# Optimization experiments

Hardware: AMD Instinct MI355X
Metric: run time of the kernel (lower is better)

## Reference

```python
import jax, jax.numpy as jnp
import numpy as np

B = 32; H = 56; W = 56; C = 384; NH = 12; WS = 7; SS = 3
N = WS * WS            # tokens per window = 49
NW = (H // WS) * (W // WS)  # windows per image = 64
HD = C // NH           # head dim = 32
MLP_H = 4 * C
EPS = 1e-5


def _rel_pos_index():
    coords = np.stack(np.meshgrid(np.arange(WS), np.arange(WS), indexing='ij'))
    cf = coords.reshape(2, -1)                      # (2, N)
    rel = cf[:, :, None] - cf[:, None, :]           # (2, N, N)
    rel = rel.transpose(1, 2, 0).astype(np.int64)   # (N, N, 2)
    rel[..., 0] += WS - 1
    rel[..., 1] += WS - 1
    rel[..., 0] *= 2 * WS - 1
    return rel.sum(-1)                               # (N, N)


def _attn_mask():
    img = np.zeros((H, W))
    cnt = 0
    slc = (slice(0, -WS), slice(-WS, -SS), slice(-SS, None))
    for hs in slc:
        for ws in slc:
            img[hs, ws] = cnt
            cnt += 1
    mw = img.reshape(H // WS, WS, W // WS, WS).transpose(0, 2, 1, 3).reshape(-1, N)  # (NW, N)
    diff = mw[:, None, :] - mw[:, :, None]
    return np.where(diff != 0, -100.0, 0.0).astype(np.float32)  # (NW, N, N)


_RPI = jnp.asarray(_rel_pos_index())
_MASK = jnp.asarray(_attn_mask())


def _ln(x, w, b):
    m = jnp.mean(x, axis=-1, keepdims=True)
    v = jnp.mean((x - m) ** 2, axis=-1, keepdims=True)
    return (x - m) * jax.lax.rsqrt(v + EPS) * w + b


def _window_partition(x):  # (B,H,W,C) -> (B*NW, WS, WS, C)
    x = x.reshape(B, H // WS, WS, W // WS, WS, C)
    return x.transpose(0, 1, 3, 2, 4, 5).reshape(-1, WS, WS, C)


def _window_reverse(xw):  # (B*NW, WS, WS, C) -> (B,H,W,C)
    x = xw.reshape(B, H // WS, W // WS, WS, WS, C)
    return x.transpose(0, 1, 3, 2, 4, 5).reshape(B, H, W, C)


def setup_inputs() -> dict:
    key = jax.random.key(0)
    ks = jax.random.split(key, 8)
    s = 0.02
    return {
        'x': jax.random.normal(ks[0], (B, H * W, C), jnp.float32),
        'norm1_w': jnp.ones((C,), jnp.float32),
        'norm1_b': jnp.zeros((C,), jnp.float32),
        'qkv_w': jax.random.normal(ks[1], (C, 3 * C), jnp.float32) * s,
        'qkv_b': jnp.zeros((3 * C,), jnp.float32),
        'rpb_table': jax.random.normal(ks[2], ((2 * WS - 1) * (2 * WS - 1), NH), jnp.float32) * s,
        'proj_w': jax.random.normal(ks[3], (C, C), jnp.float32) * s,
        'proj_b': jnp.zeros((C,), jnp.float32),
        'norm2_w': jnp.ones((C,), jnp.float32),
        'norm2_b': jnp.zeros((C,), jnp.float32),
        'fc1_w': jax.random.normal(ks[4], (C, MLP_H), jnp.float32) * s,
        'fc1_b': jnp.zeros((MLP_H,), jnp.float32),
        'fc2_w': jax.random.normal(ks[5], (MLP_H, C), jnp.float32) * s,
        'fc2_b': jnp.zeros((C,), jnp.float32),
    }


def reference(x, norm1_w, norm1_b, qkv_w, qkv_b, rpb_table, proj_w, proj_b,
              norm2_w, norm2_b, fc1_w, fc1_b, fc2_w, fc2_b):
    shortcut = x
    xn = _ln(x, norm1_w, norm1_b).reshape(B, H, W, C)
    # cyclic shift
    xs = jnp.roll(xn, shift=(-SS, -SS), axis=(1, 2))
    xw = _window_partition(xs).reshape(-1, N, C)           # (B*NW, N, C)

    qkv = (xw @ qkv_w + qkv_b).reshape(-1, N, 3, NH, HD)
    qkv = qkv.transpose(2, 0, 3, 1, 4)                      # (3, B*NW, NH, N, HD)
    q, k, v = qkv[0], qkv[1], qkv[2]
    q = q * (HD ** -0.5)
    attn = jnp.einsum('bhnd,bhmd->bhnm', q, k)              # (B*NW, NH, N, N)

    bias = rpb_table[_RPI.reshape(-1)].reshape(N, N, NH).transpose(2, 0, 1)
    attn = attn + bias[None]
    # shift mask: (NW, N, N) broadcast over batch and heads
    attn = attn.reshape(B, NW, NH, N, N) + _MASK[None, :, None]
    attn = jax.nn.softmax(attn.reshape(-1, NH, N, N), axis=-1)

    out = jnp.einsum('bhnm,bhmd->bhnd', attn, v)            # (B*NW, NH, N, HD)
    out = out.transpose(0, 2, 1, 3).reshape(-1, N, C)
    out = out @ proj_w + proj_b

    out = _window_reverse(out.reshape(-1, WS, WS, C))
    out = jnp.roll(out, shift=(SS, SS), axis=(1, 2)).reshape(B, H * W, C)

    x = shortcut + out
    h = _ln(x, norm2_w, norm2_b)
    h = jax.nn.gelu(h @ fc1_w + fc1_b, approximate=False) @ fc2_w + fc2_b
    return x + h
```

## Files before the change

### kernel.cpp

```cpp
#include <hip/hip_runtime.h>
#include <hip/hip_bf16.h>
#include <math.h>


typedef short bf16x8 __attribute__((ext_vector_type(8)));
typedef float f32x4 __attribute__((ext_vector_type(4)));

#define GLOAD_LDS16(g, s)                                                      \
    __builtin_amdgcn_global_load_lds(                                          \
        (const __attribute__((address_space(1))) void*)(g),                    \
        (__attribute__((address_space(3))) void*)(s), 16, 0, 0)

__global__ __launch_bounds__(256) void prep_k(
    const float* __restrict__ qkvw, const float* __restrict__ projw,
    const float* __restrict__ fc1w, const float* __restrict__ fc2w,
    const float* __restrict__ rpb,
    __hip_bfloat16* __restrict__ wt_qkv, __hip_bfloat16* __restrict__ wt_proj,
    __hip_bfloat16* __restrict__ wt_fc1, __hip_bfloat16* __restrict__ wt_fc2,
    float* __restrict__ biasM) {
    int id = blockIdx.x * 256 + threadIdx.x;
    if (id < 442368) {
        int k = id / 1152, n = id % 1152;
        wt_qkv[(size_t)n * 384 + k] = __float2bfloat16(qkvw[id]);
        return;
    }
    id -= 442368;
    if (id < 147456) {
        int k = id / 384, n = id % 384;
        wt_proj[(size_t)n * 384 + k] = __float2bfloat16(projw[id]);
        return;
    }
    id -= 147456;
    if (id < 589824) {
        int k = id / 1536, n = id % 1536;
        wt_fc1[(size_t)n * 384 + k] = __float2bfloat16(fc1w[id]);
        return;
    }
    id -= 589824;
    if (id < 589824) {
        int k = id / 384, n = id % 384;
        wt_fc2[(size_t)n * 1536 + k] = __float2bfloat16(fc2w[id]);
        return;
    }
    id -= 589824;
    if (id < 28812) {
        int h = id / 2401, rem = id % 2401, i = rem / 49, j = rem % 49;
        int ih = i / 7, iw = i % 7, jh = j / 7, jw = j % 7;
        int idx = (ih - jh + 6) * 13 + (iw - jw + 6);
        biasM[id] = rpb[idx * 12 + h];
    }
}

template <int MODE>
__global__ __launch_bounds__(256) void ln_k(const float* __restrict__ X,
                                            const float* __restrict__ w,
                                            const float* __restrict__ b,
                                            __hip_bfloat16* __restrict__ out) {
    int wv = threadIdx.x >> 6, lane = threadIdx.x & 63;
    int row = blockIdx.x * 4 + wv;
    size_t src_row;
    if (MODE == 0) {
        int wi = row / 49, t = row % 49;
        int bb = wi >> 6, wrem = wi & 63;
        int wh = wrem >> 3, ww = wrem & 7;
        int th = t / 7, tw = t % 7;
        int hi = (wh * 7 + th + 3) % 56;
        int wimg = (ww * 7 + tw + 3) % 56;
        src_row = (size_t)(bb * 3136 + hi * 56 + wimg);
    } else {
        src_row = row;
    }
    const float* src = X + src_row * 384;
    float v[6];
    float s = 0.f, sq = 0.f;
#pragma unroll
    for (int i = 0; i < 6; i++) {
        v[i] = src[lane + i * 64];
        s += v[i];
        sq += v[i] * v[i];
    }
#pragma unroll
    for (int m = 32; m >= 1; m >>= 1) {
        s += __shfl_xor(s, m, 64);
        sq += __shfl_xor(sq, m, 64);
    }
    float mean = s * (1.f / 384.f);
    float var = sq * (1.f / 384.f) - mean * mean;
    float rstd = rsqrtf(var + 1e-5f);
    size_t orow = (size_t)row * 384;
#pragma unroll
    for (int i = 0; i < 6; i++) {
        int c = lane + i * 64;
        out[orow + c] = __float2bfloat16((v[i] - mean) * rstd * w[c] + b[c]);
    }
}

template <int EPI>
__global__ __launch_bounds__(256) void gemm_k(
    const __hip_bfloat16* __restrict__ A, const __hip_bfloat16* __restrict__ Bt,
    const float* __restrict__ bias, int K, int nTilesN,
    __hip_bfloat16* outb, float* outf, const float* resin) {
    __shared__ __align__(16) __hip_bfloat16 Asm[2][128 * 32];
    __shared__ __align__(16) __hip_bfloat16 Bsm[2][128 * 32];
    int bid = blockIdx.x;
    int tM = bid / nTilesN, tN = bid % nTilesN;
    size_t m0 = (size_t)tM * 128;
    int n0 = tN * 128;
    int tid = threadIdx.x, wv = tid >> 6, lane = tid & 63;
    int wr = wv >> 1, wc = wv & 1;
    int lm = lane & 15, lg = lane >> 4;

    f32x4 acc[4][4];
#pragma unroll
    for (int i = 0; i < 4; i++)
#pragma unroll
        for (int j = 0; j < 4; j++) acc[i][j] = (f32x4){0.f, 0.f, 0.f, 0.f};

    int c0 = wv * 2;
    int rA0 = c0 * 16 + (lane >> 2);
    int kk = (lane & 3) * 8;
    const __hip_bfloat16* Ap = A + (m0 + rA0) * K + kk;
    const __hip_bfloat16* Bp = Bt + (size_t)(n0 + rA0) * K + kk;

    int nkt = K >> 5;
    {
        GLOAD_LDS16(Ap, &Asm[0][c0 * 512]);
        GLOAD_LDS16(Ap + (size_t)16 * K, &Asm[0][(c0 + 1) * 512]);
        GLOAD_LDS16(Bp, &Bsm[0][c0 * 512]);
        GLOAD_LDS16(Bp + (size_t)16 * K, &Bsm[0][(c0 + 1) * 512]);
    }
    for (int kt = 0; kt < nkt; kt++) {
        int cur = kt & 1;
        __syncthreads();
        if (kt + 1 < nkt) {
            int k0 = (kt + 1) << 5;
            GLOAD_LDS16(Ap + k0, &Asm[cur ^ 1][c0 * 512]);
            GLOAD_LDS16(Ap + (size_t)16 * K + k0, &Asm[cur ^ 1][(c0 + 1) * 512]);
            GLOAD_LDS16(Bp + k0, &Bsm[cur ^ 1][c0 * 512]);
            GLOAD_LDS16(Bp + (size_t)16 * K + k0, &Bsm[cur ^ 1][(c0 + 1) * 512]);
        }
        bf16x8 af[4], bfg[4];
#pragma unroll
        for (int i = 0; i < 4; i++)
            af[i] = *(const bf16x8*)&Asm[cur][(wr * 64 + i * 16 + lm) * 32 + lg * 8];
#pragma unroll
        for (int j = 0; j < 4; j++)
            bfg[j] = *(const bf16x8*)&Bsm[cur][(wc * 64 + j * 16 + lm) * 32 + lg * 8];
#pragma unroll
        for (int i = 0; i < 4; i++)
#pragma unroll
            for (int j = 0; j < 4; j++)
                acc[i][j] = __builtin_amdgcn_mfma_f32_16x16x32_bf16(
                    af[i], bfg[j], acc[i][j], 0, 0, 0);
    }

    int ld = nTilesN * 128;
#pragma unroll
    for (int i = 0; i < 4; i++) {
#pragma unroll
        for (int r = 0; r < 4; r++) {
            int row = (int)m0 + wr * 64 + i * 16 + lg * 4 + r;
#pragma unroll
            for (int j = 0; j < 4; j++) {
                int col = n0 + wc * 64 + j * 16 + lm;
                float val = acc[i][j][r] + bias[col];
                if (EPI == 0) {
                    outb[(size_t)row * ld + col] = __float2bfloat16(val);
                } else if (EPI == 2) {
                    float g = 0.5f * val * (1.f + erff(val * 0.70710678118f));
                    outb[(size_t)row * ld + col] = __float2bfloat16(g);
                } else if (EPI == 1) {
                    int wi = row / 49, t = row % 49;
                    int bb = wi >> 6, wrem = wi & 63;
                    int wh = wrem >> 3, ww = wrem & 7;
                    int th = t / 7, tw = t % 7;
                    int hi = (wh * 7 + th + 3) % 56;
                    int wimg = (ww * 7 + tw + 3) % 56;
                    size_t pos = (size_t)(bb * 3136 + hi * 56 + wimg) * 384 + col;
                    outf[pos] = resin[pos] + val;
                } else {
                    size_t pos = (size_t)row * 384 + col;
                    outf[pos] = resin[pos] + val;
                }
            }
        }
    }
}

__global__ __launch_bounds__(256) void attn_k(const __hip_bfloat16* __restrict__ qkv,
                                              const float* __restrict__ biasM,
                                              __hip_bfloat16* __restrict__ out) {
    __shared__ __align__(16) __hip_bfloat16 vt[32 * 64];
    __shared__ __align__(16) __hip_bfloat16 P[64 * 64];
    int bid = blockIdx.x;
    int wi = bid / 12, h = bid % 12;
    int tid = threadIdx.x, wv = tid >> 6, lane = tid & 63;
    int lm = lane & 15, lg = lane >> 4;
    int wrem = wi & 63, wh = wrem >> 3, ww = wrem & 7;

#pragma unroll
    for (int i = 0; i < 8; i++) vt[tid * 8 + i] = __float2bfloat16(0.f);
    __syncthreads();
    if (tid < 196) {
        int t = tid >> 2, d0 = (tid & 3) * 8;
        bf16x8 vv = *(const bf16x8*)(qkv + (size_t)(wi * 49 + t) * 1152 + 768 + h * 32 + d0);
#pragma unroll
        for (int i = 0; i < 8; i++) vt[(d0 + i) * 64 + t] = ((__hip_bfloat16*)&vv)[i];
    }

    int qrow = wv * 16 + lm;
    if (qrow > 48) qrow = 48;
    bf16x8 aq = *(const bf16x8*)(qkv + (size_t)(wi * 49 + qrow) * 1152 + h * 32 + lg * 8);
    f32x4 S[4];
#pragma unroll
    for (int ct = 0; ct < 4; ct++) {
        int krow = ct * 16 + lm;
        if (krow > 48) krow = 48;
        bf16x8 bk = *(const bf16x8*)(qkv + (size_t)(wi * 49 + krow) * 1152 + 384 + h * 32 + lg * 8);
        S[ct] = __builtin_amdgcn_mfma_f32_16x16x32_bf16(aq, bk, (f32x4){0.f, 0.f, 0.f, 0.f}, 0, 0, 0);
    }

    const float scale = 0.17677669529663687f;
#pragma unroll
    for (int r = 0; r < 4; r++) {
        int irow = wv * 16 + lg * 4 + r;
        int ic = irow <= 48 ? irow : 48;
        int ith = ic / 7, itw = ic % 7;
        int ihs = wh * 7 + ith, iws = ww * 7 + itw;
        int ridi = (ihs < 49 ? 0 : (ihs < 53 ? 1 : 2)) * 3 + (iws < 49 ? 0 : (iws < 53 ? 1 : 2));
        float vals[4];
        float mx = -1e30f;
#pragma unroll
        for (int ct = 0; ct < 4; ct++) {
            int jcol = ct * 16 + lm;
            float sv;
            if (jcol < 49) {
                int jth = jcol / 7, jtw = jcol % 7;
                int jhs = wh * 7 + jth, jws = ww * 7 + jtw;
                int ridj = (jhs < 49 ? 0 : (jhs < 53 ? 1 : 2)) * 3 + (jws < 49 ? 0 : (jws < 53 ? 1 : 2));
                sv = S[ct][r] * scale + biasM[h * 2401 + ic * 49 + jcol] +
                     (ridi != ridj ? -100.f : 0.f);
            } else {
                sv = -1e30f;
            }
            vals[ct] = sv;
            mx = fmaxf(mx, sv);
        }
#pragma unroll
        for (int m = 8; m >= 1; m >>= 1) mx = fmaxf(mx, __shfl_xor(mx, m, 64));
        float sum = 0.f;
#pragma unroll
        for (int ct = 0; ct < 4; ct++) {
            vals[ct] = __expf(vals[ct] - mx);
            sum += vals[ct];
        }
#pragma unroll
        for (int m = 8; m >= 1; m >>= 1) sum += __shfl_xor(sum, m, 64);
        float inv = 1.f / sum;
#pragma unroll
        for (int ct = 0; ct < 4; ct++)
            P[irow * 64 + ct * 16 + lm] = __float2bfloat16(vals[ct] * inv);
    }
    __syncthreads();

    f32x4 O[2] = {{0.f, 0.f, 0.f, 0.f}, {0.f, 0.f, 0.f, 0.f}};
#pragma unroll
    for (int ks = 0; ks < 2; ks++) {
        bf16x8 ap = *(const bf16x8*)&P[(wv * 16 + lm) * 64 + ks * 32 + lg * 8];
#pragma unroll
        for (int nt = 0; nt < 2; nt++) {
            bf16x8 bv = *(const bf16x8*)&vt[(nt * 16 + lm) * 64 + ks * 32 + lg * 8];
            O[nt] = __builtin_amdgcn_mfma_f32_16x16x32_bf16(ap, bv, O[nt], 0, 0, 0);
        }
    }
#pragma unroll
    for (int r = 0; r < 4; r++) {
        int row = wv * 16 + lg * 4 + r;
        if (row < 49) {
            size_t base = (size_t)(wi * 49 + row) * 384 + h * 32;
            out[base + lm] = __float2bfloat16(O[0][r]);
            out[base + 16 + lm] = __float2bfloat16(O[1][r]);
        }
    }
}

extern "C" void kernel_launch(void* const* d_in, const int* in_sizes, int n_in,
                              void* d_out, int out_size, void* d_ws, size_t ws_size,
                              hipStream_t stream) {
    (void)in_sizes; (void)n_in; (void)out_size; (void)ws_size;
    const float* x     = (const float*)d_in[0];
    const float* n1w   = (const float*)d_in[1];
    const float* n1b   = (const float*)d_in[2];
    const float* qkvw  = (const float*)d_in[3];
    const float* qkvb  = (const float*)d_in[4];
    const float* rpb   = (const float*)d_in[5];
    const float* projw = (const float*)d_in[6];
    const float* projb = (const float*)d_in[7];
    const float* n2w   = (const float*)d_in[8];
    const float* n2b   = (const float*)d_in[9];
    const float* fc1w  = (const float*)d_in[10];
    const float* fc1b  = (const float*)d_in[11];
    const float* fc2w  = (const float*)d_in[12];
    const float* fc2b  = (const float*)d_in[13];
    float* out = (float*)d_out;

    char* ws = (char*)d_ws;
    __hip_bfloat16* wt_qkv  = (__hip_bfloat16*)(ws + 0);
    __hip_bfloat16* wt_proj = (__hip_bfloat16*)(ws + 884736);
    __hip_bfloat16* wt_fc1  = (__hip_bfloat16*)(ws + 1179648);
    __hip_bfloat16* wt_fc2  = (__hip_bfloat16*)(ws + 2359296);
    float*          biasM   = (float*)(ws + 3538944);
    __hip_bfloat16* xw      = (__hip_bfloat16*)(ws + 3654656);
    __hip_bfloat16* qkv     = (__hip_bfloat16*)(ws + 80724992);
    __hip_bfloat16* attn_o  = (__hip_bfloat16*)(ws + 311936000);
    __hip_bfloat16* hidden  = xw;
    __hip_bfloat16* hn      = attn_o;

    prep_k<<<7025, 256, 0, stream>>>(qkvw, projw, fc1w, fc2w, rpb,
                                     wt_qkv, wt_proj, wt_fc1, wt_fc2, biasM);

    ln_k<0><<<25088, 256, 0, stream>>>(x, n1w, n1b, xw);
    gemm_k<0><<<784 * 9, 256, 0, stream>>>(xw, wt_qkv, qkvb, 384, 9, qkv, nullptr, nullptr);
    attn_k<<<2048 * 12, 256, 0, stream>>>(qkv, biasM, attn_o);
    gemm_k<1><<<784 * 3, 256, 0, stream>>>(attn_o, wt_proj, projb, 384, 3, nullptr, out, x);
    ln_k<1><<<25088, 256, 0, stream>>>(out, n2w, n2b, hn);
    gemm_k<2><<<784 * 12, 256, 0, stream>>>(hn, wt_fc1, fc1b, 384, 12, hidden, nullptr, nullptr);
    gemm_k<3><<<784 * 3, 256, 0, stream>>>(hidden, wt_fc2, fc2b, 1536, 3, nullptr, out, out);
}
```

Baseline: 1.327 ms.

## Triple-buffer GEMM LDS pipeline, swizzle LDS tiles, remap blocks across XCDs

```diff
diff --git a/kernel.cpp b/kernel.cpp
--- a/kernel.cpp
+++ b/kernel.cpp
@@ -100,9 +100,10 @@
     const __hip_bfloat16* __restrict__ A, const __hip_bfloat16* __restrict__ Bt,
     const float* __restrict__ bias, int K, int nTilesN,
     __hip_bfloat16* outb, float* outf, const float* resin) {
-    __shared__ __align__(16) __hip_bfloat16 Asm[2][128 * 32];
-    __shared__ __align__(16) __hip_bfloat16 Bsm[2][128 * 32];
+    __shared__ __align__(16) __hip_bfloat16 Asm[3][128 * 32];
+    __shared__ __align__(16) __hip_bfloat16 Bsm[3][128 * 32];
     int bid = blockIdx.x;
+    bid = (bid & 7) * ((int)gridDim.x >> 3) + (bid >> 3);
     int tM = bid / nTilesN, tN = bid % nTilesN;
     size_t m0 = (size_t)tM * 128;
     int n0 = tN * 128;
@@ -118,41 +119,53 @@
 
     int c0 = wv * 2;
     int rA0 = c0 * 16 + (lane >> 2);
-    int kk = (lane & 3) * 8;
+    int kk = (((lane & 3) ^ ((lane >> 3) & 3)) * 8);
     const __hip_bfloat16* Ap = A + (m0 + rA0) * K + kk;
     const __hip_bfloat16* Bp = Bt + (size_t)(n0 + rA0) * K + kk;
+    int lgs8 = (lg ^ ((lm >> 1) & 3)) * 8;
 
     int nkt = K >> 5;
-    {
-        GLOAD_LDS16(Ap, &Asm[0][c0 * 512]);
-        GLOAD_LDS16(Ap + (size_t)16 * K, &Asm[0][(c0 + 1) * 512]);
-        GLOAD_LDS16(Bp, &Bsm[0][c0 * 512]);
-        GLOAD_LDS16(Bp + (size_t)16 * K, &Bsm[0][(c0 + 1) * 512]);
-    }
+#define STAGE(buf, kt_)                                                        \
+    {                                                                          \
+        int k0_ = (kt_) << 5;                                                  \
+        GLOAD_LDS16(Ap + k0_, &Asm[buf][c0 * 512]);                            \
+        GLOAD_LDS16(Ap + (size_t)16 * K + k0_, &Asm[buf][(c0 + 1) * 512]);     \
+        GLOAD_LDS16(Bp + k0_, &Bsm[buf][c0 * 512]);                            \
+        GLOAD_LDS16(Bp + (size_t)16 * K + k0_, &Bsm[buf][(c0 + 1) * 512]);     \
+    }
+    STAGE(0, 0)
+    STAGE(1, 1)
+    int cur = 0;
     for (int kt = 0; kt < nkt; kt++) {
-        int cur = kt & 1;
-        __syncthreads();
         if (kt + 1 < nkt) {
-            int k0 = (kt + 1) << 5;
-            GLOAD_LDS16(Ap + k0, &Asm[cur ^ 1][c0 * 512]);
-            GLOAD_LDS16(Ap + (size_t)16 * K + k0, &Asm[cur ^ 1][(c0 + 1) * 512]);
-            GLOAD_LDS16(Bp + k0, &Bsm[cur ^ 1][c0 * 512]);
-            GLOAD_LDS16(Bp + (size_t)16 * K + k0, &Bsm[cur ^ 1][(c0 + 1) * 512]);
+            asm volatile("s_waitcnt vmcnt(4)" ::: "memory");
+        } else {
+            asm volatile("s_waitcnt vmcnt(0)" ::: "memory");
+        }
+        __builtin_amdgcn_s_barrier();
+        asm volatile("" ::: "memory");
+        if (kt + 2 < nkt) {
+            int b2 = cur + 2;
+            if (b2 >= 3) b2 -= 3;
+            STAGE(b2, kt + 2)
         }
         bf16x8 af[4], bfg[4];
 #pragma unroll
         for (int i = 0; i < 4; i++)
-            af[i] = *(const bf16x8*)&Asm[cur][(wr * 64 + i * 16 + lm) * 32 + lg * 8];
+            af[i] = *(const bf16x8*)&Asm[cur][(wr * 64 + i * 16 + lm) * 32 + lgs8];
 #pragma unroll
         for (int j = 0; j < 4; j++)
-            bfg[j] = *(const bf16x8*)&Bsm[cur][(wc * 64 + j * 16 + lm) * 32 + lg * 8];
+            bfg[j] = *(const bf16x8*)&Bsm[cur][(wc * 64 + j * 16 + lm) * 32 + lgs8];
 #pragma unroll
         for (int i = 0; i < 4; i++)
 #pragma unroll
             for (int j = 0; j < 4; j++)
                 acc[i][j] = __builtin_amdgcn_mfma_f32_16x16x32_bf16(
                     af[i], bfg[j], acc[i][j], 0, 0, 0);
-    }
+        cur++;
+        if (cur == 3) cur = 0;
+    }
+#undef STAGE
 
     int ld = nTilesN * 128;
 #pragma unroll
@@ -190,22 +203,23 @@
 __global__ __launch_bounds__(256) void attn_k(const __hip_bfloat16* __restrict__ qkv,
                                               const float* __restrict__ biasM,
                                               __hip_bfloat16* __restrict__ out) {
-    __shared__ __align__(16) __hip_bfloat16 vt[32 * 64];
-    __shared__ __align__(16) __hip_bfloat16 P[64 * 64];
+    __shared__ __align__(16) __hip_bfloat16 vt[32 * 72];
+    __shared__ __align__(16) __hip_bfloat16 P[64 * 72];
     int bid = blockIdx.x;
+    bid = (bid & 7) * ((int)gridDim.x >> 3) + (bid >> 3);
     int wi = bid / 12, h = bid % 12;
     int tid = threadIdx.x, wv = tid >> 6, lane = tid & 63;
     int lm = lane & 15, lg = lane >> 4;
     int wrem = wi & 63, wh = wrem >> 3, ww = wrem & 7;
 
 #pragma unroll
-    for (int i = 0; i < 8; i++) vt[tid * 8 + i] = __float2bfloat16(0.f);
+    for (int i = 0; i < 9; i++) vt[tid * 9 + i] = __float2bfloat16(0.f);
     __syncthreads();
     if (tid < 196) {
         int t = tid >> 2, d0 = (tid & 3) * 8;
         bf16x8 vv = *(const bf16x8*)(qkv + (size_t)(wi * 49 + t) * 1152 + 768 + h * 32 + d0);
 #pragma unroll
-        for (int i = 0; i < 8; i++) vt[(d0 + i) * 64 + t] = ((__hip_bfloat16*)&vv)[i];
+        for (int i = 0; i < 8; i++) vt[(d0 + i) * 72 + t] = ((__hip_bfloat16*)&vv)[i];
     }
 
     int qrow = wv * 16 + lm;
@@ -259,17 +273,17 @@
         float inv = 1.f / sum;
 #pragma unroll
         for (int ct = 0; ct < 4; ct++)
-            P[irow * 64 + ct * 16 + lm] = __float2bfloat16(vals[ct] * inv);
+            P[irow * 72 + ct * 16 + lm] = __float2bfloat16(vals[ct] * inv);
     }
     __syncthreads();
 
     f32x4 O[2] = {{0.f, 0.f, 0.f, 0.f}, {0.f, 0.f, 0.f, 0.f}};
 #pragma unroll
     for (int ks = 0; ks < 2; ks++) {
-        bf16x8 ap = *(const bf16x8*)&P[(wv * 16 + lm) * 64 + ks * 32 + lg * 8];
+        bf16x8 ap = *(const bf16x8*)&P[(wv * 16 + lm) * 72 + ks * 32 + lg * 8];
 #pragma unroll
         for (int nt = 0; nt < 2; nt++) {
-            bf16x8 bv = *(const bf16x8*)&vt[(nt * 16 + lm) * 64 + ks * 32 + lg * 8];
+            bf16x8 bv = *(const bf16x8*)&vt[(nt * 16 + lm) * 72 + ks * 32 + lg * 8];
             O[nt] = __builtin_amdgcn_mfma_f32_16x16x32_bf16(ap, bv, O[nt], 0, 0, 0);
         }
     }
```

Measured after the change: 1.306 ms. Within noise of the previous version (-1.6%).
